# Performance work log

Measured on AMD Instinct MI355X. Metric: run time of the kernel, lower is better.

Reference implementation:

```python
import jax, jax.numpy as jnp
import numpy as np
from jax import lax

N = 1000        # num_nodes
IN = 32         # in_features
H = 128         # hidden
M = 128         # message_size
DEG = 16        # regular degree
P = 2           # num_predictions
OUT = 10        # out_features
NUM_STARTS = 64


def setup_inputs() -> dict:
    key = jax.random.key(0)
    ks = jax.random.split(key, 12)
    s = 0.1
    return {
        "xa": jax.random.normal(ks[0], (N, IN), jnp.float32),
        "first_message": jax.random.normal(ks[1], (N, M), jnp.float32),
        "neighbors": jax.random.randint(ks[2], (N, DEG), 0, N, dtype=jnp.int32),
        "num_starts": NUM_STARTS,
        "enc_w": jax.random.normal(ks[3], (IN, H), jnp.float32) * s,
        "enc_b": jnp.zeros((H,), jnp.float32),
        "ns_w": jax.random.normal(ks[4], (H + M, H), jnp.float32) * s,
        "ns_b": jnp.zeros((H,), jnp.float32),
        "nm_w": jax.random.normal(ks[5], (H + M, M), jnp.float32) * s,
        "nm_b": jnp.zeros((M,), jnp.float32),
        "act_w": jax.random.normal(ks[6], (H + M, 1), jnp.float32) * s,
        "act_b": jnp.zeros((1,), jnp.float32),
        "dec_w": jax.random.normal(ks[7], (P, H, OUT), jnp.float32) * s,
        "dec_b": jnp.zeros((P, OUT), jnp.float32),
    }


def reference(xa, first_message, neighbors, num_starts,
              enc_w, enc_b, ns_w, ns_b, nm_w, nm_b, act_w, act_b, dec_w, dec_b):
    n = xa.shape[0]
    deg = neighbors.shape[1]
    m = first_message.shape[1]
    max_msgs = 10 * n                      # messages < num_nodes * 10 cap
    cap = num_starts + max_msgs * deg      # max queue size (static)

    feats0 = xa @ enc_w + enc_b            # encoder, latest state per node
    qn = jnp.zeros((cap,), jnp.int32).at[:num_starts].set(
        jnp.arange(num_starts, dtype=jnp.int32))
    qm = jnp.zeros((cap, m), feats0.dtype).at[:num_starts].set(
        first_message[:num_starts])

    carry = (jnp.int32(0), jnp.int32(num_starts), qn, qm,
             feats0, jnp.zeros_like(feats0), jnp.zeros((n,), feats0.dtype))

    def step(c, _):
        head, tail, qn, qm, feats, final, tact = c
        active = head < tail                          # queue nonempty
        node = qn[head]
        msg = lax.dynamic_slice(qm, (head, 0), (1, m))[0]
        ta = tact[node]
        proc = active & (ta <= 1.0 - 1e-7)            # ACT halting check
        f = feats[node]
        x = jnp.concatenate([f, msg])                 # [H+M]
        cand = jax.nn.sigmoid(x @ act_w + act_b)[0]
        new_act = jnp.where(ta + cand > 1.0, 1.0 - ta, cand)
        ns = jax.nn.relu(x @ ns_w + ns_b)             # new state [H]
        nm_ = jnp.concatenate([ns, msg]) @ nm_w + nm_b  # new message [M]
        # enqueue deg neighbor messages (gated write)
        old_n = lax.dynamic_slice(qn, (tail,), (deg,))
        old_m = lax.dynamic_slice(qm, (tail, 0), (deg, m))
        qn = lax.dynamic_update_slice(
            qn, jnp.where(proc, neighbors[node], old_n), (tail,))
        qm = lax.dynamic_update_slice(
            qm, jnp.where(proc, jnp.broadcast_to(nm_, (deg, m)), old_m), (tail, 0))
        feats = feats.at[node].set(jnp.where(proc, ns, f))
        final = final.at[node].add(jnp.where(proc, ns * new_act, 0.0))
        tact = tact.at[node].add(jnp.where(proc, new_act, 0.0))
        head = head + active.astype(jnp.int32)
        tail = tail + proc.astype(jnp.int32) * deg
        return (head, tail, qn, qm, feats, final, tact), None

    (_, _, _, _, _, final, _), _ = lax.scan(step, carry, None, length=max_msgs)

    g = jnp.sum(final, axis=0, keepdims=True)          # graph_class readout [1,H]
    logits = jnp.einsum('nh,pho->pno', g, dec_w) + dec_b[:, None, :]
    return jax.nn.log_softmax(logits, axis=-1)         # [P, 1, OUT]
```

## Files before the change

kernel.cpp:

```cpp
#include <hip/hip_runtime.h>
#include <math.h>

#define NN 1000
#define INF_ 32
#define H 128
#define M 128
#define DEG 16
#define PP 2
#define OUTF 10
#define MAXM (10 * NN)
#define QCAP (MAXM + DEG)
#define NSLOT (MAXM + 128)
#define NT 512
#define WQ (2 * NT)
#define WROW 264
#define NROW 136

typedef _Float16 half8 __attribute__((ext_vector_type(8)));
typedef float floatx4 __attribute__((ext_vector_type(4)));

__device__ __forceinline__ void bar_lds() {
    asm volatile("s_waitcnt lgkmcnt(0)\n\ts_barrier" ::: "memory");
}


__global__ __launch_bounds__(128)
void init_kernel(const float* __restrict__ xa, const float* __restrict__ fm,
                 const float* __restrict__ enc_w, const float* __restrict__ enc_b,
                 const int* __restrict__ nstart_p,
                 _Float16* __restrict__ feats_h, float* __restrict__ finalv,
                 _Float16* __restrict__ nmbuf_h) {
    int b = blockIdx.x, t = threadIdx.x;
    float acc = enc_b[t];
    const float* xr = xa + b * INF_;
#pragma unroll
    for (int k = 0; k < INF_; ++k) acc += xr[k] * enc_w[k * H + t];
    feats_h[b * H + t] = (_Float16)acc;
    finalv[b * H + t] = 0.0f;
    if (b < nstart_p[0]) nmbuf_h[(size_t)b * M + t] = (_Float16)fm[b * M + t];
}

__global__ __launch_bounds__(256)
void pack_kernel(const float* __restrict__ ns_w, const float* __restrict__ nm_w,
                 _Float16* __restrict__ wnsB, _Float16* __restrict__ wnmB) {
    const int idx = blockIdx.x * 256 + threadIdx.x;
    if (idx >= 128 * WROW) return;
    const int n = idx / WROW, k = idx % WROW;
    wnsB[idx] = (k < 256) ? (_Float16)ns_w[k * H + n] : (_Float16)0.0f;
    wnmB[idx] = (k < 256) ? (_Float16)nm_w[k * M + n] : (_Float16)0.0f;
}

__global__ __launch_bounds__(NT, 1)
void seq_kernel(const int* __restrict__ neighbors,
                const float* __restrict__ ns_b, const float* __restrict__ nm_b,
                const float* __restrict__ act_w, const float* __restrict__ act_b,
                const float* __restrict__ dec_w, const float* __restrict__ dec_b,
                const int* __restrict__ nstart_p,
                const _Float16* __restrict__ wnsB, const _Float16* __restrict__ wnmB,
                _Float16* __restrict__ feats_h, float* __restrict__ finalv,
                _Float16* __restrict__ nmbuf_h, unsigned int* __restrict__ qpack_unused,
                float* __restrict__ out) {
    __shared__ __align__(16) _Float16 s_Xh[2][16 * WROW];
    __shared__ __align__(16) _Float16 s_NSh[2][16 * NROW];
    __shared__ unsigned int s_q[QCAP];
    __shared__ float s_tact[NN];
    __shared__ int   s_mark[NN];
    __shared__ float s_actw[H + M];
    __shared__ float s_nsb[H];
    __shared__ float s_nmb[M];
    __shared__ float s_rna[2][16];
    __shared__ unsigned short s_rns[2 * WQ];
    __shared__ unsigned int  s_enq[WQ];
    __shared__ unsigned char s_flag[NT];
    __shared__ int s_wc[8], s_wd[8];
    __shared__ int s_cnt;

    unsigned short* const s_rnode = s_rns;
    unsigned short* const s_rslot = s_rns + WQ;
    short* s_order = (short*)s_mark;
    float* s_g  = (float*)(s_mark + 512);
    float* s_lg = (float*)(s_mark + 512 + 128);

    const int t = threadIdx.x;
    const int lane = t & 63, wid = t >> 6;
    const int quad = lane >> 4, lm = lane & 15;
    const int colw = (wid << 4) + lm;
    const int sg = t & 31;
    const int r16 = t >> 5, c8 = t & 31;
    const int nstart = nstart_p[0];
    const int rsoff = (c8 < 16) ? 0 : WQ;
    const _Float16* const gsrc = (c8 < 16) ? (feats_h + c8 * 8)
                                           : (nmbuf_h + (c8 - 16) * 8);

    half8 wbn[8], wbm[8];
#pragma unroll
    for (int c = 0; c < 8; ++c) {
        wbn[c] = *(const half8*)(wnsB + (size_t)colw * WROW + (c << 5) + (quad << 3));
        wbm[c] = *(const half8*)(wnmB + (size_t)colw * WROW + (c << 5) + (quad << 3));
    }

    for (int i = t; i < NN; i += NT) { s_tact[i] = 0.0f; s_mark[i] = 0x7fffffff; }
    for (int i = t; i < nstart; i += NT) s_q[i] = (unsigned)i | ((unsigned)i << 16);
    if (t < H + M) s_actw[t] = act_w[t];
    if (t < H) { s_nsb[t] = ns_b[t]; s_nmb[t] = nm_b[t]; }
    const float actb = act_b[0];
    __syncthreads();
    const float nsb_c = s_nsb[colw];
    const float nmb_c = s_nmb[colw];
    float aw[8];
#pragma unroll
    for (int j = 0; j < 8; ++j) aw[j] = s_actw[sg * 8 + j];

    int head = 0, tail = nstart, gbase = nstart;
    for (;;) {
        const int lim = min(tail, MAXM);
        if (head >= lim) break;
        const int W = min(WQ, lim - head);

        int nodeA = 0, slotA = 0; bool remA = false;
        int nodeB = 0, slotB = 0; bool remB = false;
        if (t < W) {
            const unsigned v = s_q[head + t];
            nodeA = (int)(v & 0xffffu);
            slotA = (int)(v >> 16);
            remA = (s_tact[nodeA] <= 1.0f - 1e-7f);
        }
        if (NT + t < W) {
            const unsigned v = s_q[head + NT + t];
            nodeB = (int)(v & 0xffffu);
            slotB = (int)(v >> 16);
            remB = (s_tact[nodeB] <= 1.0f - 1e-7f);
        }
        s_flag[t] = 0;
        s_mark[t] = 0x7fffffff;
        bar_lds();

        int base = 0;
        for (;;) {
            const bool rem2a = remA && (s_tact[nodeA] <= 1.0f - 1e-7f);
            const bool rem2b = remB && (s_tact[nodeB] <= 1.0f - 1e-7f);
            if (rem2a) atomicMin(&s_mark[nodeA], t);
            if (rem2b) atomicMin(&s_mark[nodeB], NT + t);
            if (t == 0) s_cnt = 0;
            bar_lds();
            const bool winA = rem2a && (s_mark[nodeA] == t);
            const bool winB = rem2b && (s_mark[nodeB] == NT + t);
            const unsigned long long ma = __ballot(winA);
            const unsigned long long mb = __ballot(winB);
            const int ca = __popcll(ma), cb = __popcll(mb);
            int wbase = 0;
            if (lane == 0 && (ca + cb)) wbase = atomicAdd(&s_cnt, ca + cb);
            wbase = __shfl(wbase, 0, 64);
            const unsigned long long below = (1ull << lane) - 1ull;
            if (winA) {
                const int wrank = wbase + __popcll(ma & below);
                s_rnode[wrank] = (unsigned short)nodeA;
                s_rslot[wrank] = (unsigned short)slotA;
                s_enq[t] = (unsigned)nodeA | ((unsigned)(gbase + base + wrank) << 16);
                s_flag[t] |= 1;
            }
            if (winB) {
                const int wrank = wbase + ca + __popcll(mb & below);
                s_rnode[wrank] = (unsigned short)nodeB;
                s_rslot[wrank] = (unsigned short)slotB;
                s_enq[NT + t] = (unsigned)nodeB | ((unsigned)(gbase + base + wrank) << 16);
                s_flag[t] |= 2;
            }
            remA = rem2a && !winA;
            remB = rem2b && !winB;
            bar_lds();
            if (rem2a) s_mark[nodeA] = 0x7fffffff;
            if (rem2b) s_mark[nodeB] = 0x7fffffff;
            const int Pr = s_cnt;
            if (Pr == 0) break;

            uint4 px = *(const uint4*)(gsrc + (size_t)s_rns[rsoff + min(r16, Pr - 1)] * 128);
            *(uint4*)(s_Xh[0] + r16 * WROW + (c8 << 3)) = px;
            float zredC;
            {
                const half8 hv = *(const half8*)&px;
                float p = 0.0f;
#pragma unroll
                for (int j = 0; j < 8; ++j) p += (float)hv[j] * aw[j];
#pragma unroll
                for (int off = 16; off > 0; off >>= 1) p += __shfl_down(p, off, 32);
                zredC = p;
            }
            if (Pr > 16)
                px = *(const uint4*)(gsrc + (size_t)s_rns[rsoff + min(16 + r16, Pr - 1)] * 128);
            bar_lds();

            floatx4 accmP = {0.0f, 0.0f, 0.0f, 0.0f};
            float nsvP[4] = {0, 0, 0, 0};
            int   nrP[4] = {0, 0, 0, 0};
            int PcP = 0, sbP = 0;

            for (int c0 = 0; c0 < Pr; c0 += 16) {
                const int k = c0 >> 4;
                const int cur = k & 1, nxt = cur ^ 1;
                const int rem = Pr - c0;
                const bool fullC = rem >= 16;
                const int Pc = fullC ? 16 : rem;
                const bool hasnext = rem > 16;
                float zredN = 0.0f;
                if (hasnext) {
                    *(uint4*)(s_Xh[nxt] + r16 * WROW + (c8 << 3)) = px;
                    const half8 hv = *(const half8*)&px;
                    float p = 0.0f;
#pragma unroll
                    for (int j = 0; j < 8; ++j) p += (float)hv[j] * aw[j];
#pragma unroll
                    for (int off = 16; off > 0; off >>= 1) p += __shfl_down(p, off, 32);
                    zredN = p;
                }
                if (rem > 32)
                    px = *(const uint4*)(gsrc + (size_t)s_rns[rsoff + min(c0 + 32 + r16, Pr - 1)] * 128);
                int nrC[4];
                if (fullC) {
#pragma unroll
                    for (int i = 0; i < 4; ++i)
                        nrC[i] = (int)s_rnode[c0 + (quad << 2) + i];
                } else {
#pragma unroll
                    for (int i = 0; i < 4; ++i)
                        nrC[i] = (int)s_rnode[min(c0 + (quad << 2) + i, Pr - 1)];
                }
                if (c0 > 0) {
                    const _Float16* nrow = s_NSh[nxt] + lm * NROW + (quad << 3);
#pragma unroll
                    for (int c = 0; c < 4; ++c)
                        accmP = __builtin_amdgcn_mfma_f32_16x16x32_f16(
                            *(const half8*)(nrow + (c << 5)), wbm[c], accmP, 0, 0, 0);
                    float na4[4];
#pragma unroll
                    for (int i = 0; i < 4; ++i) na4[i] = s_rna[nxt][(quad << 2) + i];
                    if (PcP == 16) {
#pragma unroll
                        for (int i = 0; i < 4; ++i)
                            nmbuf_h[(size_t)(sbP + (quad << 2) + i) * M + colw] =
                                (_Float16)(accmP[i] + nmb_c);
#pragma unroll
                        for (int i = 0; i < 4; ++i)
                            atomicAdd(finalv + (size_t)nrP[i] * H + colw,
                                      nsvP[i] * na4[i]);
                    } else {
#pragma unroll
                        for (int i = 0; i < 4; ++i) {
                            const int r = (quad << 2) + i;
                            if (r < PcP) {
                                nmbuf_h[(size_t)(sbP + r) * M + colw] =
                                    (_Float16)(accmP[i] + nmb_c);
                                atomicAdd(finalv + (size_t)nrP[i] * H + colw,
                                          nsvP[i] * na4[i]);
                            }
                        }
                    }
                }
                if (sg == 0 && r16 < Pc) {
                    const float z = zredC + actb;
                    const float cnd = 1.0f / (1.0f + expf(-z));
                    const int nr = (int)s_rnode[c0 + r16];
                    const float ta = s_tact[nr];
                    const float na = (ta + cnd > 1.0f) ? (1.0f - ta) : cnd;
                    s_rna[cur][r16] = na;
                    s_tact[nr] = ta + na;
                }
                floatx4 accn = {0.0f, 0.0f, 0.0f, 0.0f};
                floatx4 accm = {0.0f, 0.0f, 0.0f, 0.0f};
                {
                    const _Float16* xrow = s_Xh[cur] + lm * WROW + (quad << 3);
                    half8 a[8];
#pragma unroll
                    for (int c = 0; c < 8; ++c) a[c] = *(const half8*)(xrow + (c << 5));
#pragma unroll
                    for (int c = 0; c < 8; ++c)
                        accn = __builtin_amdgcn_mfma_f32_16x16x32_f16(
                            a[c], wbn[c], accn, 0, 0, 0);
#pragma unroll
                    for (int c = 4; c < 8; ++c)
                        accm = __builtin_amdgcn_mfma_f32_16x16x32_f16(
                            a[c], wbm[c], accm, 0, 0, 0);
                }
                float nsv[4];
#pragma unroll
                for (int i = 0; i < 4; ++i) nsv[i] = fmaxf(accn[i] + nsb_c, 0.0f);
                if (fullC) {
#pragma unroll
                    for (int i = 0; i < 4; ++i) {
                        const int r = (quad << 2) + i;
                        s_NSh[cur][r * NROW + colw] = (_Float16)nsv[i];
                        feats_h[(size_t)nrC[i] * H + colw] = (_Float16)nsv[i];
                    }
                } else {
#pragma unroll
                    for (int i = 0; i < 4; ++i) {
                        const int r = (quad << 2) + i;
                        if (r < Pc) {
                            s_NSh[cur][r * NROW + colw] = (_Float16)nsv[i];
                            feats_h[(size_t)nrC[i] * H + colw] = (_Float16)nsv[i];
                        }
                    }
                }
                accmP = accm;
#pragma unroll
                for (int i = 0; i < 4; ++i) { nsvP[i] = nsv[i]; nrP[i] = nrC[i]; }
                PcP = Pc; sbP = gbase + base + c0;
                zredC = zredN;
                bar_lds();
            }
            {
                const int pb = ((Pr - 1) >> 4) & 1;
                const _Float16* nrow = s_NSh[pb] + lm * NROW + (quad << 3);
#pragma unroll
                for (int c = 0; c < 4; ++c)
                    accmP = __builtin_amdgcn_mfma_f32_16x16x32_f16(
                        *(const half8*)(nrow + (c << 5)), wbm[c], accmP, 0, 0, 0);
                float na4[4];
#pragma unroll
                for (int i = 0; i < 4; ++i) na4[i] = s_rna[pb][(quad << 2) + i];
#pragma unroll
                for (int i = 0; i < 4; ++i) {
                    const int r = (quad << 2) + i;
                    if (r < PcP) {
                        nmbuf_h[(size_t)(sbP + r) * M + colw] =
                            (_Float16)(accmP[i] + nmb_c);
                        atomicAdd(finalv + (size_t)nrP[i] * H + colw,
                                  nsvP[i] * na4[i]);
                    }
                }
            }
            base += Pr;
            __syncthreads();
        }

        const bool pfa = (s_flag[t] & 1) != 0;
        const bool pfb = (s_flag[t] & 2) != 0;
        const unsigned long long mfa = __ballot(pfa);
        const unsigned long long mfb = __ballot(pfb);
        if (lane == 0) { s_wc[wid] = __popcll(mfa); s_wd[wid] = __popcll(mfb); }
        bar_lds();
        int TA = 0, TB = 0, preA = 0, preB = 0;
#pragma unroll
        for (int w = 0; w < 8; ++w) {
            TA += s_wc[w]; TB += s_wd[w];
            preA += (w < wid) ? s_wc[w] : 0;
            preB += (w < wid) ? s_wd[w] : 0;
        }
        const int T = TA + TB;
        if (T > 0) {
            const unsigned long long below = (1ull << lane) - 1ull;
            if (pfa) s_order[preA + __popcll(mfa & below)] = (short)t;
            if (pfb) s_order[TA + preB + __popcll(mfb & below)] = (short)(NT + t);
            bar_lds();
            for (int idx = t; idx < T * DEG; idx += NT) {
                const int e = (int)s_order[idx >> 4];
                const unsigned v = s_enq[e];
                const int nd = (int)(v & 0xffffu);
                const unsigned slot = v >> 16;
                const int q = tail + idx;
                if (q < QCAP)
                    s_q[q] = (unsigned)neighbors[nd * DEG + (idx & 15)] | (slot << 16);
            }
        }
        tail += DEG * T;
        gbase += T;
        head += W;
        bar_lds();
    }

    if (t < H) {
        float g0 = 0, g1 = 0, g2 = 0, g3 = 0;
        for (int n = 0; n < NN; n += 4) {
            g0 += finalv[(n + 0) * H + t];
            g1 += finalv[(n + 1) * H + t];
            g2 += finalv[(n + 2) * H + t];
            g3 += finalv[(n + 3) * H + t];
        }
        s_g[t] = (g0 + g1) + (g2 + g3);
    }
    __syncthreads();
    if (t < PP * OUTF) {
        const int pp = t / OUTF, o = t % OUTF;
        float acc = dec_b[pp * OUTF + o];
        for (int h = 0; h < H; ++h) acc += s_g[h] * dec_w[(pp * H + h) * OUTF + o];
        s_lg[t] = acc;
    }
    __syncthreads();
    if (t < PP * OUTF) {
        const int pp = t / OUTF;
        float mx = -INFINITY;
        for (int o = 0; o < OUTF; ++o) mx = fmaxf(mx, s_lg[pp * OUTF + o]);
        float s = 0.0f;
        for (int o = 0; o < OUTF; ++o) s += expf(s_lg[pp * OUTF + o] - mx);
        out[t] = s_lg[t] - (mx + logf(s));
    }
}

extern "C" void kernel_launch(void* const* d_in, const int* in_sizes, int n_in,
                              void* d_out, int out_size, void* d_ws, size_t ws_size,
                              hipStream_t stream) {
    const float* xa        = (const float*)d_in[0];
    const float* fm        = (const float*)d_in[1];
    const int*   neighbors = (const int*)  d_in[2];
    const int*   nstart_p  = (const int*)  d_in[3];
    const float* enc_w     = (const float*)d_in[4];
    const float* enc_b     = (const float*)d_in[5];
    const float* ns_w      = (const float*)d_in[6];
    const float* ns_b      = (const float*)d_in[7];
    const float* nm_w      = (const float*)d_in[8];
    const float* nm_b      = (const float*)d_in[9];
    const float* act_w     = (const float*)d_in[10];
    const float* act_b     = (const float*)d_in[11];
    const float* dec_w     = (const float*)d_in[12];
    const float* dec_b     = (const float*)d_in[13];
    float* out = (float*)d_out;

    char* w = (char*)d_ws;
    _Float16* feats_h = (_Float16*)w;                 w += (size_t)NN * H * 2;
    float*    finalv  = (float*)w;                    w += (size_t)NN * H * 4;
    _Float16* nmbuf_h = (_Float16*)w;                 w += (size_t)NSLOT * M * 2;
    _Float16* wnsB    = (_Float16*)w;                 w += (size_t)128 * WROW * 2;
    _Float16* wnmB    = (_Float16*)w;                 w += (size_t)128 * WROW * 2;
    unsigned int* qpack = (unsigned int*)w;

    init_kernel<<<NN, 128, 0, stream>>>(xa, fm, enc_w, enc_b, nstart_p,
                                        feats_h, finalv, nmbuf_h);
    pack_kernel<<<132, 256, 0, stream>>>(ns_w, nm_w, wnsB, wnmB);
    seq_kernel<<<1, NT, 0, stream>>>(neighbors, ns_b, nm_b,
                                     act_w, act_b, dec_w, dec_b, nstart_p,
                                     wnsB, wnmB,
                                     feats_h, finalv, nmbuf_h, qpack, out);
}
```

Measured before the change: 548.2 us.

## Process 32 winner rows per pipelined chunk with dual MFMA tiles

Doubles the per-iteration row chunk in the sequential message-processing loop from 16 to 32 rows. Two 16-row MFMA tiles are computed per chunk, with doubled LDS staging buffers and two prefetched rows per thread. This halves the number of chunk iterations and their barriers, and exposes more independent MFMA work per step. In exchange it uses more registers and LDS, and adds waste when the winner count per round is small. It also replaces the per-round __syncthreads with an explicit vmcnt wait plus an LDS barrier.

After: 554.2 us. About the same (+1.1%).

```diff
diff --git a/kernel.cpp b/kernel.cpp
--- a/kernel.cpp
+++ b/kernel.cpp
@@ -23,7 +23,6 @@
     asm volatile("s_waitcnt lgkmcnt(0)\n\ts_barrier" ::: "memory");
 }
 
-
 __global__ __launch_bounds__(128)
 void init_kernel(const float* __restrict__ xa, const float* __restrict__ fm,
                  const float* __restrict__ enc_w, const float* __restrict__ enc_b,
@@ -60,15 +59,15 @@
                 _Float16* __restrict__ feats_h, float* __restrict__ finalv,
                 _Float16* __restrict__ nmbuf_h, unsigned int* __restrict__ qpack_unused,
                 float* __restrict__ out) {
-    __shared__ __align__(16) _Float16 s_Xh[2][16 * WROW];
-    __shared__ __align__(16) _Float16 s_NSh[2][16 * NROW];
+    __shared__ __align__(16) _Float16 s_Xh[2][32 * WROW];
+    __shared__ __align__(16) _Float16 s_NSh[2][32 * NROW];
     __shared__ unsigned int s_q[QCAP];
     __shared__ float s_tact[NN];
     __shared__ int   s_mark[NN];
     __shared__ float s_actw[H + M];
     __shared__ float s_nsb[H];
     __shared__ float s_nmb[M];
-    __shared__ float s_rna[2][16];
+    __shared__ float s_rna[2][32];
     __shared__ unsigned short s_rns[2 * WQ];
     __shared__ unsigned int  s_enq[WQ];
     __shared__ unsigned char s_flag[NT];
@@ -76,7 +75,6 @@
     __shared__ int s_cnt;
 
     unsigned short* const s_rnode = s_rns;
-    unsigned short* const s_rslot = s_rns + WQ;
     short* s_order = (short*)s_mark;
     float* s_g  = (float*)(s_mark + 512);
     float* s_lg = (float*)(s_mark + 512 + 128);
@@ -84,6 +82,7 @@
     const int t = threadIdx.x;
     const int lane = t & 63, wid = t >> 6;
     const int quad = lane >> 4, lm = lane & 15;
+    const int q4 = quad << 2;
     const int colw = (wid << 4) + lm;
     const int sg = t & 31;
     const int r16 = t >> 5, c8 = t & 31;
@@ -110,6 +109,16 @@
     float aw[8];
 #pragma unroll
     for (int j = 0; j < 8; ++j) aw[j] = s_actw[sg * 8 + j];
+
+    auto gate = [&](uint4 v) -> float {
+        const half8 hv = *(const half8*)&v;
+        float p = 0.0f;
+#pragma unroll
+        for (int j = 0; j < 8; ++j) p += (float)hv[j] * aw[j];
+#pragma unroll
+        for (int off = 16; off > 0; off >>= 1) p += __shfl_down(p, off, 32);
+        return p;
+    };
 
     int head = 0, tail = nstart, gbase = nstart;
     for (;;) {
@@ -142,6 +151,7 @@
             if (rem2a) atomicMin(&s_mark[nodeA], t);
             if (rem2b) atomicMin(&s_mark[nodeB], NT + t);
             if (t == 0) s_cnt = 0;
+            asm volatile("s_waitcnt vmcnt(0)" ::: "memory");
             bar_lds();
             const bool winA = rem2a && (s_mark[nodeA] == t);
             const bool winB = rem2b && (s_mark[nodeB] == NT + t);
@@ -154,15 +164,15 @@
             const unsigned long long below = (1ull << lane) - 1ull;
             if (winA) {
                 const int wrank = wbase + __popcll(ma & below);
-                s_rnode[wrank] = (unsigned short)nodeA;
-                s_rslot[wrank] = (unsigned short)slotA;
+                s_rns[wrank] = (unsigned short)nodeA;
+                s_rns[WQ + wrank] = (unsigned short)slotA;
                 s_enq[t] = (unsigned)nodeA | ((unsigned)(gbase + base + wrank) << 16);
                 s_flag[t] |= 1;
             }
             if (winB) {
                 const int wrank = wbase + ca + __popcll(mb & below);
-                s_rnode[wrank] = (unsigned short)nodeB;
-                s_rslot[wrank] = (unsigned short)slotB;
+                s_rns[wrank] = (unsigned short)nodeB;
+                s_rns[WQ + wrank] = (unsigned short)slotB;
                 s_enq[NT + t] = (unsigned)nodeB | ((unsigned)(gbase + base + wrank) << 16);
                 s_flag[t] |= 2;
             }
@@ -174,163 +184,231 @@
             const int Pr = s_cnt;
             if (Pr == 0) break;
 
-            uint4 px = *(const uint4*)(gsrc + (size_t)s_rns[rsoff + min(r16, Pr - 1)] * 128);
-            *(uint4*)(s_Xh[0] + r16 * WROW + (c8 << 3)) = px;
-            float zredC;
-            {
-                const half8 hv = *(const half8*)&px;
-                float p = 0.0f;
-#pragma unroll
-                for (int j = 0; j < 8; ++j) p += (float)hv[j] * aw[j];
-#pragma unroll
-                for (int off = 16; off > 0; off >>= 1) p += __shfl_down(p, off, 32);
-                zredC = p;
+            uint4 pxL = *(const uint4*)(gsrc + (size_t)s_rns[rsoff + min(r16, Pr - 1)] * 128);
+            uint4 pxU = *(const uint4*)(gsrc + (size_t)s_rns[rsoff + min(16 + r16, Pr - 1)] * 128);
+            *(uint4*)(s_Xh[0] + r16 * WROW + (c8 << 3)) = pxL;
+            *(uint4*)(s_Xh[0] + (16 + r16) * WROW + (c8 << 3)) = pxU;
+            float zredCL = gate(pxL);
+            float zredCU = gate(pxU);
+            if (Pr > 32) {
+                pxL = *(const uint4*)(gsrc + (size_t)s_rns[rsoff + min(32 + r16, Pr - 1)] * 128);
+                pxU = *(const uint4*)(gsrc + (size_t)s_rns[rsoff + min(48 + r16, Pr - 1)] * 128);
             }
-            if (Pr > 16)
-                px = *(const uint4*)(gsrc + (size_t)s_rns[rsoff + min(16 + r16, Pr - 1)] * 128);
             bar_lds();
 
-            floatx4 accmP = {0.0f, 0.0f, 0.0f, 0.0f};
-            float nsvP[4] = {0, 0, 0, 0};
-            int   nrP[4] = {0, 0, 0, 0};
-            int PcP = 0, sbP = 0;
-
-            for (int c0 = 0; c0 < Pr; c0 += 16) {
-                const int k = c0 >> 4;
+            floatx4 accmPL = {0, 0, 0, 0}, accmPU = {0, 0, 0, 0};
+            float nsvPL[4] = {0, 0, 0, 0}, nsvPU[4] = {0, 0, 0, 0};
+            int   nrPL[4] = {0, 0, 0, 0}, nrPU[4] = {0, 0, 0, 0};
+            int PcPL = 0, PcPU = 0, sbP = 0;
+
+            for (int c0 = 0; c0 < Pr; c0 += 32) {
+                const int k = c0 >> 5;
                 const int cur = k & 1, nxt = cur ^ 1;
-                const int rem = Pr - c0;
-                const bool fullC = rem >= 16;
-                const int Pc = fullC ? 16 : rem;
-                const bool hasnext = rem > 16;
-                float zredN = 0.0f;
+                const int remn = Pr - c0;
+                const bool fullU = remn >= 32;
+                const int PcL = (remn >= 16) ? 16 : remn;
+                const int PcU = fullU ? 16 : (remn > 16 ? remn - 16 : 0);
+                const bool hasnext = remn > 32;
+                float zredNL = 0.0f, zredNU = 0.0f;
                 if (hasnext) {
-                    *(uint4*)(s_Xh[nxt] + r16 * WROW + (c8 << 3)) = px;
-                    const half8 hv = *(const half8*)&px;
-                    float p = 0.0f;
-#pragma unroll
-                    for (int j = 0; j < 8; ++j) p += (float)hv[j] * aw[j];
-#pragma unroll
-                    for (int off = 16; off > 0; off >>= 1) p += __shfl_down(p, off, 32);
-                    zredN = p;
-                }
-                if (rem > 32)
-                    px = *(const uint4*)(gsrc + (size_t)s_rns[rsoff + min(c0 + 32 + r16, Pr - 1)] * 128);
-                int nrC[4];
-                if (fullC) {
-#pragma unroll
-                    for (int i = 0; i < 4; ++i)
-                        nrC[i] = (int)s_rnode[c0 + (quad << 2) + i];
+                    *(uint4*)(s_Xh[nxt] + r16 * WROW + (c8 << 3)) = pxL;
+                    *(uint4*)(s_Xh[nxt] + (16 + r16) * WROW + (c8 << 3)) = pxU;
+                    zredNL = gate(pxL);
+                    zredNU = gate(pxU);
+                }
+                if (remn > 64) {
+                    pxL = *(const uint4*)(gsrc + (size_t)s_rns[rsoff + min(c0 + 64 + r16, Pr - 1)] * 128);
+                    pxU = *(const uint4*)(gsrc + (size_t)s_rns[rsoff + min(c0 + 80 + r16, Pr - 1)] * 128);
+                }
+                int nrL[4], nrU[4];
+                if (fullU) {
+#pragma unroll
+                    for (int i = 0; i < 4; ++i) {
+                        nrL[i] = (int)s_rnode[c0 + q4 + i];
+                        nrU[i] = (int)s_rnode[c0 + 16 + q4 + i];
+                    }
                 } else {
 #pragma unroll
-                    for (int i = 0; i < 4; ++i)
-                        nrC[i] = (int)s_rnode[min(c0 + (quad << 2) + i, Pr - 1)];
+                    for (int i = 0; i < 4; ++i) {
+                        nrL[i] = (int)s_rnode[min(c0 + q4 + i, Pr - 1)];
+                        nrU[i] = (int)s_rnode[min(c0 + 16 + q4 + i, Pr - 1)];
+                    }
                 }
                 if (c0 > 0) {
-                    const _Float16* nrow = s_NSh[nxt] + lm * NROW + (quad << 3);
-#pragma unroll
-                    for (int c = 0; c < 4; ++c)
-                        accmP = __builtin_amdgcn_mfma_f32_16x16x32_f16(
-                            *(const half8*)(nrow + (c << 5)), wbm[c], accmP, 0, 0, 0);
-                    float na4[4];
-#pragma unroll
-                    for (int i = 0; i < 4; ++i) na4[i] = s_rna[nxt][(quad << 2) + i];
-                    if (PcP == 16) {
-#pragma unroll
-                        for (int i = 0; i < 4; ++i)
-                            nmbuf_h[(size_t)(sbP + (quad << 2) + i) * M + colw] =
-                                (_Float16)(accmP[i] + nmb_c);
-#pragma unroll
-                        for (int i = 0; i < 4; ++i)
-                            atomicAdd(finalv + (size_t)nrP[i] * H + colw,
-                                      nsvP[i] * na4[i]);
+                    {
+                        const _Float16* nrow = s_NSh[nxt] + lm * NROW + (quad << 3);
+#pragma unroll
+                        for (int c = 0; c < 4; ++c)
+                            accmPL = __builtin_amdgcn_mfma_f32_16x16x32_f16(
+                                *(const half8*)(nrow + (c << 5)), wbm[c], accmPL, 0, 0, 0);
+                    }
+                    {
+                        const _Float16* nrow = s_NSh[nxt] + (16 + lm) * NROW + (quad << 3);
+#pragma unroll
+                        for (int c = 0; c < 4; ++c)
+                            accmPU = __builtin_amdgcn_mfma_f32_16x16x32_f16(
+                                *(const half8*)(nrow + (c << 5)), wbm[c], accmPU, 0, 0, 0);
+                    }
+                    float naL[4], naU[4];
+#pragma unroll
+                    for (int i = 0; i < 4; ++i) {
+                        naL[i] = s_rna[nxt][q4 + i];
+                        naU[i] = s_rna[nxt][16 + q4 + i];
+                    }
+                    if (PcPU == 16) {
+#pragma unroll
+                        for (int i = 0; i < 4; ++i) {
+                            nmbuf_h[(size_t)(sbP + q4 + i) * M + colw] =
+                                (_Float16)(accmPL[i] + nmb_c);
+                            nmbuf_h[(size_t)(sbP + 16 + q4 + i) * M + colw] =
+                                (_Float16)(accmPU[i] + nmb_c);
+                        }
+#pragma unroll
+                        for (int i = 0; i < 4; ++i) {
+                            atomicAdd(finalv + (size_t)nrPL[i] * H + colw, nsvPL[i] * naL[i]);
+                            atomicAdd(finalv + (size_t)nrPU[i] * H + colw, nsvPU[i] * naU[i]);
+                        }
                     } else {
 #pragma unroll
                         for (int i = 0; i < 4; ++i) {
-                            const int r = (quad << 2) + i;
-                            if (r < PcP) {
+                            const int r = q4 + i;
+                            if (r < PcPL) {
                                 nmbuf_h[(size_t)(sbP + r) * M + colw] =
-                                    (_Float16)(accmP[i] + nmb_c);
-                                atomicAdd(finalv + (size_t)nrP[i] * H + colw,
-                                          nsvP[i] * na4[i]);
+                                    (_Float16)(accmPL[i] + nmb_c);
+                                atomicAdd(finalv + (size_t)nrPL[i] * H + colw,
+                                          nsvPL[i] * naL[i]);
+                            }
+                            if (r < PcPU) {
+                                nmbuf_h[(size_t)(sbP + 16 + r) * M + colw] =
+                                    (_Float16)(accmPU[i] + nmb_c);
+                                atomicAdd(finalv + (size_t)nrPU[i] * H + colw,
+                                          nsvPU[i] * naU[i]);
                             }
                         }
                     }
                 }
-                if (sg == 0 && r16 < Pc) {
-                    const float z = zredC + actb;
-                    const float cnd = 1.0f / (1.0f + expf(-z));
-                    const int nr = (int)s_rnode[c0 + r16];
-                    const float ta = s_tact[nr];
-                    const float na = (ta + cnd > 1.0f) ? (1.0f - ta) : cnd;
-                    s_rna[cur][r16] = na;
-                    s_tact[nr] = ta + na;
-                }
-                floatx4 accn = {0.0f, 0.0f, 0.0f, 0.0f};
-                floatx4 accm = {0.0f, 0.0f, 0.0f, 0.0f};
+                if (sg == 0) {
+                    if (r16 < PcL) {
+                        const float z = zredCL + actb;
+                        const float cnd = 1.0f / (1.0f + expf(-z));
+                        const int nr = (int)s_rnode[c0 + r16];
+                        const float ta = s_tact[nr];
+                        const float na = (ta + cnd > 1.0f) ? (1.0f - ta) : cnd;
+                        s_rna[cur][r16] = na;
+                        s_tact[nr] = ta + na;
+                    }
+                    if (r16 < PcU) {
+                        const float z = zredCU + actb;
+                        const float cnd = 1.0f / (1.0f + expf(-z));
+                        const int nr = (int)s_rnode[c0 + 16 + r16];
+                        const float ta = s_tact[nr];
+                        const float na = (ta + cnd > 1.0f) ? (1.0f - ta) : cnd;
+                        s_rna[cur][16 + r16] = na;
+                        s_tact[nr] = ta + na;
+                    }
+                }
+                floatx4 accmL, accmU;
+                float nsvL[4], nsvU[4];
                 {
+                    floatx4 accn = {0, 0, 0, 0}, accm = {0, 0, 0, 0};
                     const _Float16* xrow = s_Xh[cur] + lm * WROW + (quad << 3);
                     half8 a[8];
 #pragma unroll
                     for (int c = 0; c < 8; ++c) a[c] = *(const half8*)(xrow + (c << 5));
 #pragma unroll
                     for (int c = 0; c < 8; ++c)
-                        accn = __builtin_amdgcn_mfma_f32_16x16x32_f16(
-                            a[c], wbn[c], accn, 0, 0, 0);
+                        accn = __builtin_amdgcn_mfma_f32_16x16x32_f16(a[c], wbn[c], accn, 0, 0, 0);
 #pragma unroll
                     for (int c = 4; c < 8; ++c)
-                        accm = __builtin_amdgcn_mfma_f32_16x16x32_f16(
-                            a[c], wbm[c], accm, 0, 0, 0);
-                }
-                float nsv[4];
-#pragma unroll
-                for (int i = 0; i < 4; ++i) nsv[i] = fmaxf(accn[i] + nsb_c, 0.0f);
-                if (fullC) {
+                        accm = __builtin_amdgcn_mfma_f32_16x16x32_f16(a[c], wbm[c], accm, 0, 0, 0);
+#pragma unroll
+                    for (int i = 0; i < 4; ++i) nsvL[i] = fmaxf(accn[i] + nsb_c, 0.0f);
+                    accmL = accm;
+                }
+                {
+                    floatx4 accn = {0, 0, 0, 0}, accm = {0, 0, 0, 0};
+                    const _Float16* xrow = s_Xh[cur] + (16 + lm) * WROW + (quad << 3);
+                    half8 a[8];
+#pragma unroll
+                    for (int c = 0; c < 8; ++c) a[c] = *(const half8*)(xrow + (c << 5));
+#pragma unroll
+                    for (int c = 0; c < 8; ++c)
+                        accn = __builtin_amdgcn_mfma_f32_16x16x32_f16(a[c], wbn[c], accn, 0, 0, 0);
+#pragma unroll
+                    for (int c = 4; c < 8; ++c)
+                        accm = __builtin_amdgcn_mfma_f32_16x16x32_f16(a[c], wbm[c], accm, 0, 0, 0);
+#pragma unroll
+                    for (int i = 0; i < 4; ++i) nsvU[i] = fmaxf(accn[i] + nsb_c, 0.0f);
+                    accmU = accm;
+                }
+                if (fullU) {
 #pragma unroll
                     for (int i = 0; i < 4; ++i) {
-                        const int r = (quad << 2) + i;
-                        s_NSh[cur][r * NROW + colw] = (_Float16)nsv[i];
-                        feats_h[(size_t)nrC[i] * H + colw] = (_Float16)nsv[i];
+                        const int r = q4 + i;
+                        s_NSh[cur][r * NROW + colw] = (_Float16)nsvL[i];
+                        feats_h[(size_t)nrL[i] * H + colw] = (_Float16)nsvL[i];
+                        s_NSh[cur][(16 + r) * NROW + colw] = (_Float16)nsvU[i];
+                        feats_h[(size_t)nrU[i] * H + colw] = (_Float16)nsvU[i];
                     }
                 } else {
 #pragma unroll
                     for (int i = 0; i < 4; ++i) {
-                        const int r = (quad << 2) + i;
-                        if (r < Pc) {
-                            s_NSh[cur][r * NROW + colw] = (_Float16)nsv[i];
-                            feats_h[(size_t)nrC[i] * H + colw] = (_Float16)nsv[i];
+                        const int r = q4 + i;
+                        if (r < PcL) {
+                            s_NSh[cur][r * NROW + colw] = (_Float16)nsvL[i];
+                            feats_h[(size_t)nrL[i] * H + colw] = (_Float16)nsvL[i];
                         }
-                    }
-                }
-                accmP = accm;
-#pragma unroll
-                for (int i = 0; i < 4; ++i) { nsvP[i] = nsv[i]; nrP[i] = nrC[i]; }
-                PcP = Pc; sbP = gbase + base + c0;
-                zredC = zredN;
+                        if (r < PcU) {
+                            s_NSh[cur][(16 + r) * NROW + colw] = (_Float16)nsvU[i];
+                            feats_h[(size_t)nrU[i] * H + colw] = (_Float16)nsvU[i];
+                        }
+                    }
+                }
+                accmPL = accmL; accmPU = accmU;
+#pragma unroll
+                for (int i = 0; i < 4; ++i) {
+                    nsvPL[i] = nsvL[i]; nrPL[i] = nrL[i];
+                    nsvPU[i] = nsvU[i]; nrPU[i] = nrU[i];
+                }
+                PcPL = PcL; PcPU = PcU; sbP = gbase + base + c0;
+                zredCL = zredNL; zredCU = zredNU;
                 bar_lds();
             }
             {
-                const int pb = ((Pr - 1) >> 4) & 1;
-                const _Float16* nrow = s_NSh[pb] + lm * NROW + (quad << 3);
-#pragma unroll
-                for (int c = 0; c < 4; ++c)
-                    accmP = __builtin_amdgcn_mfma_f32_16x16x32_f16(
-                        *(const half8*)(nrow + (c << 5)), wbm[c], accmP, 0, 0, 0);
-                float na4[4];
-#pragma unroll
-                for (int i = 0; i < 4; ++i) na4[i] = s_rna[pb][(quad << 2) + i];
+                const int pb = ((Pr - 1) >> 5) & 1;
+                {
+                    const _Float16* nrow = s_NSh[pb] + lm * NROW + (quad << 3);
+#pragma unroll
+                    for (int c = 0; c < 4; ++c)
+                        accmPL = __builtin_amdgcn_mfma_f32_16x16x32_f16(
+                            *(const half8*)(nrow + (c << 5)), wbm[c], accmPL, 0, 0, 0);
+                }
+                {
+                    const _Float16* nrow = s_NSh[pb] + (16 + lm) * NROW + (quad << 3);
+#pragma unroll
+                    for (int c = 0; c < 4; ++c)
+                        accmPU = __builtin_amdgcn_mfma_f32_16x16x32_f16(
+                            *(const half8*)(nrow + (c << 5)), wbm[c], accmPU, 0, 0, 0);
+                }
 #pragma unroll
                 for (int i = 0; i < 4; ++i) {
-                    const int r = (quad << 2) + i;
-                    if (r < PcP) {
+                    const int r = q4 + i;
+                    if (r < PcPL) {
                         nmbuf_h[(size_t)(sbP + r) * M + colw] =
-                            (_Float16)(accmP[i] + nmb_c);
-                        atomicAdd(finalv + (size_t)nrP[i] * H + colw,
-                                  nsvP[i] * na4[i]);
+                            (_Float16)(accmPL[i] + nmb_c);
+                        atomicAdd(finalv + (size_t)nrPL[i] * H + colw,
+                                  nsvPL[i] * s_rna[pb][r]);
+                    }
+                    if (r < PcPU) {
+                        nmbuf_h[(size_t)(sbP + 16 + r) * M + colw] =
+                            (_Float16)(accmPU[i] + nmb_c);
+                        atomicAdd(finalv + (size_t)nrPU[i] * H + colw,
+                                  nsvPU[i] * s_rna[pb][16 + r]);
                     }
                 }
             }
             base += Pr;
-            __syncthreads();
+            bar_lds();
         }
 
         const bool pfa = (s_flag[t] & 1) != 0;
@@ -367,6 +445,8 @@
         head += W;
         bar_lds();
     }
+
+    __syncthreads();
 
     if (t < H) {
         float g0 = 0, g1 = 0, g2 = 0, g3 = 0;
```
